# Optimization experiments

Hardware: AMD Instinct MI355X
Metric: run time of the kernel (lower is better)

Reference implementation:

```python
import jax, jax.numpy as jnp
import numpy as np

B, H, WD = 4, 1440, 1440      # batch, BEV grid (sparse_shape)
N, C, NB = 200000, 32, 3      # active voxels, channels, num basic blocks
EPS = 1e-3                    # BatchNorm1d eps in the module


def setup_inputs() -> dict:
    key = jax.random.key(0)
    ks = jax.random.split(key, 10)
    feats = jax.random.normal(ks[0], (N, C), jnp.float32)
    coords_b = jax.random.randint(ks[1], (N,), 0, B, dtype=jnp.int32)
    coords_y = jax.random.randint(ks[2], (N,), 0, H, dtype=jnp.int32)
    coords_x = jax.random.randint(ks[3], (N,), 0, WD, dtype=jnp.int32)
    # [block, conv(2), tap(3x3=9), Cin, Cout]; fan-in scaled init
    Wk = jax.random.normal(ks[4], (NB, 2, 9, C, C), jnp.float32) / np.sqrt(9 * C)
    bias = 0.01 * jax.random.normal(ks[5], (NB, 2, C), jnp.float32)
    gamma = 1.0 + 0.1 * jax.random.normal(ks[6], (NB, 2, C), jnp.float32)
    beta = 0.1 * jax.random.normal(ks[7], (NB, 2, C), jnp.float32)
    mean = 0.1 * jax.random.normal(ks[8], (NB, 2, C), jnp.float32)
    var = jax.random.uniform(ks[9], (NB, 2, C), jnp.float32, 0.5, 1.5)
    return dict(feats=feats, Wk=Wk, bias=bias, gamma=gamma, beta=beta,
                mean=mean, var=var, coords_b=coords_b, coords_y=coords_y,
                coords_x=coords_x)


def _build_rulebook(coords_b, coords_y, coords_x):
    # Dense hash: grid cell -> voxel row id (-1 if empty). Shared by all
    # submanifold convs in the stage (same indice_key in the original).
    idx_map = jnp.full((B, H, WD), -1, jnp.int32)
    idx_map = idx_map.at[coords_b, coords_y, coords_x].set(
        jnp.arange(N, dtype=jnp.int32))
    offs = jnp.array([(dy, dx) for dy in (-1, 0, 1) for dx in (-1, 0, 1)],
                     jnp.int32)                      # [9,2]
    ny = coords_y[None, :] + offs[:, 0:1]            # [9,N]
    nx = coords_x[None, :] + offs[:, 1:2]
    inb = (ny >= 0) & (ny < H) & (nx >= 0) & (nx < WD)
    nyc = jnp.clip(ny, 0, H - 1)
    nxc = jnp.clip(nx, 0, WD - 1)
    nidx = idx_map[jnp.broadcast_to(coords_b[None, :], (9, N)), nyc, nxc]
    mask = inb & (nidx >= 0)
    nidx = jnp.where(mask, nidx, 0)                  # safe gather index
    return nidx, mask[..., None].astype(jnp.float32)


def reference(feats, Wk, bias, gamma, beta, mean, var,
              coords_b, coords_y, coords_x):
    nidx, maskf = _build_rulebook(coords_b, coords_y, coords_x)

    def subm(x, w, b):
        # gather-GEMM-scatter submanifold 3x3 conv on active sites only
        g = x[nidx] * maskf                          # [9,N,Cin]
        return jnp.einsum('knc,kco->no', g, w) + b   # [N,Cout]

    def bn(x, g_, b_, m_, v_):
        return (x - m_) * jax.lax.rsqrt(v_ + EPS) * g_ + b_

    h = feats
    for i in range(NB):  # SparseBasicBlock stack (fixed small layer count)
        identity = h
        o = jax.nn.relu(bn(subm(h, Wk[i, 0], bias[i, 0]),
                           gamma[i, 0], beta[i, 0], mean[i, 0], var[i, 0]))
        o = bn(subm(o, Wk[i, 1], bias[i, 1]),
               gamma[i, 1], beta[i, 1], mean[i, 1], var[i, 1])
        h = jax.nn.relu(o + identity)
    return h
```

## Files before the change

kernel.cpp:

```cpp
#include <hip/hip_runtime.h>

#define NB_ 3
#define CB 4
#define CH 1440
#define CW 1440
#define NC 32
#define EPSV 1e-3f

typedef __attribute__((ext_vector_type(8))) short bf16x8;
typedef __attribute__((ext_vector_type(4))) float f32x4;

union U16 { uint4 u; bf16x8 v; };

__device__ __forceinline__ unsigned pk2(float a, float b) {
    unsigned ua = __float_as_uint(a), ub = __float_as_uint(b);
    ua += 0x7fffu + ((ua >> 16) & 1u);
    ub += 0x7fffu + ((ub >> 16) & 1u);
    return (ua >> 16) | (ub & 0xffff0000u);
}
__device__ __forceinline__ unsigned short f2b(float a) {
    unsigned u = __float_as_uint(a);
    u += 0x7fffu + ((u >> 16) & 1u);
    return (unsigned short)(u >> 16);
}
__device__ __forceinline__ float b2f(unsigned short s) {
    return __uint_as_float(((unsigned)s) << 16);
}

__global__ __launch_bounds__(256) void k_clear(
    const int* __restrict__ cb, const int* __restrict__ cy, const int* __restrict__ cx,
    int* __restrict__ idx_map, int n)
{
    int i = blockIdx.x * blockDim.x + threadIdx.x;
    if (i >= n) return;
    int b = cb[i], y = cy[i], x = cx[i];
    #pragma unroll
    for (int dy = -1; dy <= 1; ++dy) {
        int yy = y + dy;
        if (yy < 0 || yy >= CH) continue;
        #pragma unroll
        for (int dx = -1; dx <= 1; ++dx) {
            int xx = x + dx;
            if (xx < 0 || xx >= CW) continue;
            idx_map[((long)b * CH + yy) * CW + xx] = -1;
        }
    }
}

__global__ __launch_bounds__(256) void k_build_map(
    const int* __restrict__ cb, const int* __restrict__ cy, const int* __restrict__ cx,
    int* __restrict__ idx_map, int n)
{
    int i = blockIdx.x * blockDim.x + threadIdx.x;
    if (i < n) {
        long cell = ((long)cb[i] * CH + cy[i]) * CW + cx[i];
        atomicMax(&idx_map[cell], i);
    }
}

__global__ __launch_bounds__(256) void k_rulebook(
    const int* __restrict__ cb, const int* __restrict__ cy, const int* __restrict__ cx,
    const int* __restrict__ idx_map, int* __restrict__ nidx, int n)
{
    int i = blockIdx.x * blockDim.x + threadIdx.x;
    if (i >= n) return;
    int b = cb[i], y = cy[i], x = cx[i];
    nidx[4 * n + i] = idx_map[((long)b * CH + y) * CW + x];
    #pragma unroll
    for (int k = 0; k < 9; ++k) {
        if (k == 4) continue;
        int dy = k / 3 - 1, dx = k % 3 - 1;
        int ny = y + dy, nx = x + dx;
        int nb = -1;
        if (ny >= 0 && ny < CH && nx >= 0 && nx < CW)
            nb = idx_map[((long)b * CH + ny) * CW + nx];
        nidx[k * n + i] = nb;
    }
}

__global__ __launch_bounds__(256) void k_cvt(
    const float* __restrict__ f, unsigned short* __restrict__ b, int n32)
{
    int i = (blockIdx.x * 256 + threadIdx.x) * 8;
    if (i + 8 <= n32) {
        float4 a0 = *(const float4*)(f + i);
        float4 a1 = *(const float4*)(f + i + 4);
        uint4 r;
        r.x = pk2(a0.x, a0.y); r.y = pk2(a0.z, a0.w);
        r.z = pk2(a1.x, a1.y); r.w = pk2(a1.z, a1.w);
        *(uint4*)(b + i) = r;
    }
}

template<bool ADD_ID, bool F32OUT>
__global__ __launch_bounds__(256, 4) void k_conv(
    const unsigned short* __restrict__ in,
    const unsigned short* __restrict__ idn,
    void* __restrict__ outv,
    const float* __restrict__ W,
    const float* __restrict__ bias,
    const float* __restrict__ gamma, const float* __restrict__ beta,
    const float* __restrict__ mean, const float* __restrict__ var,
    const int* __restrict__ nidx, int n)
{
    __shared__ uint4 Bf[9 * 2 * 64];

    int tid = threadIdx.x;
    int l = tid & 63, wv = tid >> 6;

    for (int t = tid; t < 9 * 2 * 64; t += 256) {
        int lane = t & 63, nt = (t >> 6) & 1, k = t >> 7;
        int o = nt * 16 + (lane & 15);
        int c0 = (lane >> 4) * 8;
        const float* wp = W + k * 1024 + o;
        uint4 r;
        r.x = pk2(wp[(c0 + 0) * 32], wp[(c0 + 1) * 32]);
        r.y = pk2(wp[(c0 + 2) * 32], wp[(c0 + 3) * 32]);
        r.z = pk2(wp[(c0 + 4) * 32], wp[(c0 + 5) * 32]);
        r.w = pk2(wp[(c0 + 6) * 32], wp[(c0 + 7) * 32]);
        Bf[t] = r;
    }
    __syncthreads();

    int row = l & 15, grp = l >> 4;
    int o0 = row, o1 = row + 16;

    float sc0 = gamma[o0] * rsqrtf(var[o0] + EPSV);
    float sh0 = (bias[o0] - mean[o0]) * sc0 + beta[o0];
    float sc1 = gamma[o1] * rsqrtf(var[o1] + EPSV);
    float sh1 = (bias[o1] - mean[o1]) * sc1 + beta[o1];

    int ntile = (n + 15) >> 4;
    for (int tile = blockIdx.x * 4 + wv; tile < ntile; tile += gridDim.x * 4) {
        int p0 = tile << 4;
        int pr = p0 + row;
        bool rowok = pr < n;
        int prc = rowok ? pr : n - 1;

        int idxk[9];
        #pragma unroll
        for (int k = 0; k < 9; ++k) idxk[k] = nidx[(size_t)k * n + prc];

        bool act[9];
        U16 a[9];
        #pragma unroll
        for (int k = 0; k < 9; ++k) {
            act[k] = __any(idxk[k] >= 0);
            if (act[k]) {
                bool valid = rowok && (idxk[k] >= 0);
                int si = valid ? idxk[k] : 0;
                uint4 r = *(const uint4*)(in + (size_t)si * 32 + grp * 8);
                a[k].u.x = valid ? r.x : 0u;
                a[k].u.y = valid ? r.y : 0u;
                a[k].u.z = valid ? r.z : 0u;
                a[k].u.w = valid ? r.w : 0u;
            }
        }

        f32x4 acc0 = {0.f, 0.f, 0.f, 0.f};
        f32x4 acc1 = {0.f, 0.f, 0.f, 0.f};
        #pragma unroll
        for (int k = 0; k < 9; ++k) {
            if (act[k]) {
                U16 b0, b1;
                b0.u = Bf[(k * 2 + 0) * 64 + l];
                b1.u = Bf[(k * 2 + 1) * 64 + l];
                acc0 = __builtin_amdgcn_mfma_f32_16x16x32_bf16(a[k].v, b0.v, acc0, 0, 0, 0);
                acc1 = __builtin_amdgcn_mfma_f32_16x16x32_bf16(a[k].v, b1.v, acc1, 0, 0, 0);
            }
        }

        #pragma unroll
        for (int r = 0; r < 4; ++r) {
            int p = p0 + grp * 4 + r;
            if (p < n) {
                float y0 = acc0[r] * sc0 + sh0;
                float y1 = acc1[r] * sc1 + sh1;
                if (ADD_ID) {
                    y0 += b2f(idn[(size_t)p * 32 + o0]);
                    y1 += b2f(idn[(size_t)p * 32 + o1]);
                }
                y0 = fmaxf(y0, 0.f);
                y1 = fmaxf(y1, 0.f);
                if (F32OUT) {
                    ((float*)outv)[(size_t)p * 32 + o0] = y0;
                    ((float*)outv)[(size_t)p * 32 + o1] = y1;
                } else {
                    ((unsigned short*)outv)[(size_t)p * 32 + o0] = f2b(y0);
                    ((unsigned short*)outv)[(size_t)p * 32 + o1] = f2b(y1);
                }
            }
        }
    }
}

extern "C" void kernel_launch(void* const* d_in, const int* in_sizes, int n_in,
                              void* d_out, int out_size, void* d_ws, size_t ws_size,
                              hipStream_t stream)
{
    const float* feats = (const float*)d_in[0];
    const float* Wk    = (const float*)d_in[1];
    const float* bias  = (const float*)d_in[2];
    const float* gamma = (const float*)d_in[3];
    const float* beta  = (const float*)d_in[4];
    const float* mean  = (const float*)d_in[5];
    const float* var   = (const float*)d_in[6];
    const int* cb = (const int*)d_in[7];
    const int* cy = (const int*)d_in[8];
    const int* cx = (const int*)d_in[9];
    float* out = (float*)d_out;
    int n = in_sizes[0] / NC;

    char* ws = (char*)d_ws;
    int*            idx_map = (int*)(ws + 0);
    int*            nidx    = (int*)(ws + 33177600);
    unsigned short* xbf     = (unsigned short*)(ws + 40441600);
    unsigned short* tmpbf   = (unsigned short*)(ws + 53241600);
    unsigned short* hb      = (unsigned short*)(ws + 66041600);

    int blocks = (n + 255) / 256;
    k_clear<<<blocks, 256, 0, stream>>>(cb, cy, cx, idx_map, n);
    k_build_map<<<blocks, 256, 0, stream>>>(cb, cy, cx, idx_map, n);
    k_rulebook<<<blocks, 256, 0, stream>>>(cb, cy, cx, idx_map, nidx, n);
    k_cvt<<<(n * NC / 8 + 255) / 256, 256, 0, stream>>>(feats, xbf, n * NC);

    const int G = 1024;
    const int WSZ = 9 * 32 * 32;

    k_conv<false, false><<<G, 256, 0, stream>>>(xbf, nullptr, tmpbf,
        Wk + 0 * WSZ, bias + 0,  gamma + 0,  beta + 0,  mean + 0,  var + 0,  nidx, n);
    k_conv<true,  false><<<G, 256, 0, stream>>>(tmpbf, xbf, hb,
        Wk + 1 * WSZ, bias + 32, gamma + 32, beta + 32, mean + 32, var + 32, nidx, n);
    k_conv<false, false><<<G, 256, 0, stream>>>(hb, nullptr, tmpbf,
        Wk + 2 * WSZ, bias + 64, gamma + 64, beta + 64, mean + 64, var + 64, nidx, n);
    k_conv<true,  false><<<G, 256, 0, stream>>>(tmpbf, hb, xbf,
        Wk + 3 * WSZ, bias + 96, gamma + 96, beta + 96, mean + 96, var + 96, nidx, n);
    k_conv<false, false><<<G, 256, 0, stream>>>(xbf, nullptr, tmpbf,
        Wk + 4 * WSZ, bias + 128, gamma + 128, beta + 128, mean + 128, var + 128, nidx, n);
    k_conv<true,  true><<<G, 256, 0, stream>>>(tmpbf, xbf, out,
        Wk + 5 * WSZ, bias + 160, gamma + 160, beta + 160, mean + 160, var + 160, nidx, n);
}
```

Measured before the change: 149.5 us.

## Switch conv to 32x32x16 MFMA tiles with precomputed bf16 weights and byte offsets

Each conv kernel now works on 32-row tiles with the 32x32x16 bf16 MFMA instead of two 16x16x32 MFMAs on 16-row tiles. Weights for all six layers are converted to bf16 fragment layout once in a separate kernel and read from global memory, so each conv block no longer rebuilds them in shared memory. The rulebook now stores byte offsets, and a zero row appended to each feature buffer replaces the per-element select masking. The gathers are interleaved with the MFMAs. In exchange, the accumulator grows to 16 floats per lane, which raises register pressure, and the epilogue stores become more strided.

```diff
diff --git a/kernel.cpp b/kernel.cpp
--- a/kernel.cpp
+++ b/kernel.cpp
@@ -8,7 +8,7 @@
 #define EPSV 1e-3f
 
 typedef __attribute__((ext_vector_type(8))) short bf16x8;
-typedef __attribute__((ext_vector_type(4))) float f32x4;
+typedef __attribute__((ext_vector_type(16))) float f32x16;
 
 union U16 { uint4 u; bf16x8 v; };
 
@@ -60,12 +60,12 @@
 
 __global__ __launch_bounds__(256) void k_rulebook(
     const int* __restrict__ cb, const int* __restrict__ cy, const int* __restrict__ cx,
-    const int* __restrict__ idx_map, int* __restrict__ nidx, int n)
+    const int* __restrict__ idx_map, int* __restrict__ roff, int n)
 {
     int i = blockIdx.x * blockDim.x + threadIdx.x;
     if (i >= n) return;
     int b = cb[i], y = cy[i], x = cx[i];
-    nidx[4 * n + i] = idx_map[((long)b * CH + y) * CW + x];
+    roff[4 * n + i] = idx_map[((long)b * CH + y) * CW + x] * 64;
     #pragma unroll
     for (int k = 0; k < 9; ++k) {
         if (k == 4) continue;
@@ -74,7 +74,7 @@
         int nb = -1;
         if (ny >= 0 && ny < CH && nx >= 0 && nx < CW)
             nb = idx_map[((long)b * CH + ny) * CW + nx];
-        nidx[k * n + i] = nb;
+        roff[k * n + i] = (nb >= 0) ? nb * 64 : -1;
     }
 }
 
@@ -92,103 +92,90 @@
     }
 }
 
+__global__ __launch_bounds__(256) void k_wcvt(
+    const float* __restrict__ Wk, uint4* __restrict__ Bfg,
+    unsigned short* __restrict__ z0, unsigned short* __restrict__ z1,
+    unsigned short* __restrict__ z2)
+{
+    if (blockIdx.x == 0 && threadIdx.x < 12) {
+        uint4 z = make_uint4(0, 0, 0, 0);
+        int tt = threadIdx.x;
+        if (tt < 4)       ((uint4*)z0)[tt] = z;
+        else if (tt < 8)  ((uint4*)z1)[tt - 4] = z;
+        else              ((uint4*)z2)[tt - 8] = z;
+    }
+    int t = blockIdx.x * 256 + threadIdx.x;
+    if (t >= 6 * 9 * 2 * 64) return;
+    int l = t & 63, h = (t >> 6) & 1;
+    int rest = t >> 7;
+    int k = rest % 9, layer = rest / 9;
+    int o = l & 31;
+    int c0 = h * 16 + 8 * (l >> 5);
+    const float* wp = Wk + (size_t)layer * 9216 + k * 1024 + o;
+    uint4 r;
+    r.x = pk2(wp[(c0 + 0) * 32], wp[(c0 + 1) * 32]);
+    r.y = pk2(wp[(c0 + 2) * 32], wp[(c0 + 3) * 32]);
+    r.z = pk2(wp[(c0 + 4) * 32], wp[(c0 + 5) * 32]);
+    r.w = pk2(wp[(c0 + 6) * 32], wp[(c0 + 7) * 32]);
+    Bfg[t] = r;
+}
+
 template<bool ADD_ID, bool F32OUT>
 __global__ __launch_bounds__(256, 4) void k_conv(
     const unsigned short* __restrict__ in,
     const unsigned short* __restrict__ idn,
     void* __restrict__ outv,
-    const float* __restrict__ W,
+    const uint4* __restrict__ Bf,
     const float* __restrict__ bias,
     const float* __restrict__ gamma, const float* __restrict__ beta,
     const float* __restrict__ mean, const float* __restrict__ var,
-    const int* __restrict__ nidx, int n)
-{
-    __shared__ uint4 Bf[9 * 2 * 64];
-
-    int tid = threadIdx.x;
-    int l = tid & 63, wv = tid >> 6;
-
-    for (int t = tid; t < 9 * 2 * 64; t += 256) {
-        int lane = t & 63, nt = (t >> 6) & 1, k = t >> 7;
-        int o = nt * 16 + (lane & 15);
-        int c0 = (lane >> 4) * 8;
-        const float* wp = W + k * 1024 + o;
-        uint4 r;
-        r.x = pk2(wp[(c0 + 0) * 32], wp[(c0 + 1) * 32]);
-        r.y = pk2(wp[(c0 + 2) * 32], wp[(c0 + 3) * 32]);
-        r.z = pk2(wp[(c0 + 4) * 32], wp[(c0 + 5) * 32]);
-        r.w = pk2(wp[(c0 + 6) * 32], wp[(c0 + 7) * 32]);
-        Bf[t] = r;
-    }
-    __syncthreads();
-
-    int row = l & 15, grp = l >> 4;
-    int o0 = row, o1 = row + 16;
-
-    float sc0 = gamma[o0] * rsqrtf(var[o0] + EPSV);
-    float sh0 = (bias[o0] - mean[o0]) * sc0 + beta[o0];
-    float sc1 = gamma[o1] * rsqrtf(var[o1] + EPSV);
-    float sh1 = (bias[o1] - mean[o1]) * sc1 + beta[o1];
-
-    int ntile = (n + 15) >> 4;
+    const int* __restrict__ roff, int n)
+{
+    int l = threadIdx.x & 63, wv = threadIdx.x >> 6;
+    int q = l & 31, h5 = l >> 5;
+
+    float sc = gamma[q] * rsqrtf(var[q] + EPSV);
+    float sh = (bias[q] - mean[q]) * sc + beta[q];
+
+    const int zoff = n * 64;
+    const char* inB = (const char*)in;
+
+    int ntile = (n + 31) >> 5;
     for (int tile = blockIdx.x * 4 + wv; tile < ntile; tile += gridDim.x * 4) {
-        int p0 = tile << 4;
-        int pr = p0 + row;
+        int p0 = tile << 5;
+        int pr = p0 + q;
         bool rowok = pr < n;
         int prc = rowok ? pr : n - 1;
 
-        int idxk[9];
-        #pragma unroll
-        for (int k = 0; k < 9; ++k) idxk[k] = nidx[(size_t)k * n + prc];
-
-        bool act[9];
-        U16 a[9];
+        int rk[9];
+        #pragma unroll
+        for (int k = 0; k < 9; ++k) rk[k] = roff[(size_t)k * n + prc];
+
+        f32x16 acc = {0.f,0.f,0.f,0.f,0.f,0.f,0.f,0.f,0.f,0.f,0.f,0.f,0.f,0.f,0.f,0.f};
         #pragma unroll
         for (int k = 0; k < 9; ++k) {
-            act[k] = __any(idxk[k] >= 0);
-            if (act[k]) {
-                bool valid = rowok && (idxk[k] >= 0);
-                int si = valid ? idxk[k] : 0;
-                uint4 r = *(const uint4*)(in + (size_t)si * 32 + grp * 8);
-                a[k].u.x = valid ? r.x : 0u;
-                a[k].u.y = valid ? r.y : 0u;
-                a[k].u.z = valid ? r.z : 0u;
-                a[k].u.w = valid ? r.w : 0u;
+            if (__any(rk[k] >= 0)) {
+                int off = (rowok && rk[k] >= 0) ? rk[k] : zoff;
+                const char* ap = inB + off + h5 * 16;
+                U16 a0, a1, b0, b1;
+                a0.u = *(const uint4*)(ap);
+                a1.u = *(const uint4*)(ap + 32);
+                b0.u = Bf[(k * 2 + 0) * 64 + l];
+                b1.u = Bf[(k * 2 + 1) * 64 + l];
+                acc = __builtin_amdgcn_mfma_f32_32x32x16_bf16(a0.v, b0.v, acc, 0, 0, 0);
+                acc = __builtin_amdgcn_mfma_f32_32x32x16_bf16(a1.v, b1.v, acc, 0, 0, 0);
             }
         }
 
-        f32x4 acc0 = {0.f, 0.f, 0.f, 0.f};
-        f32x4 acc1 = {0.f, 0.f, 0.f, 0.f};
-        #pragma unroll
-        for (int k = 0; k < 9; ++k) {
-            if (act[k]) {
-                U16 b0, b1;
-                b0.u = Bf[(k * 2 + 0) * 64 + l];
-                b1.u = Bf[(k * 2 + 1) * 64 + l];
-                acc0 = __builtin_amdgcn_mfma_f32_16x16x32_bf16(a[k].v, b0.v, acc0, 0, 0, 0);
-                acc1 = __builtin_amdgcn_mfma_f32_16x16x32_bf16(a[k].v, b1.v, acc1, 0, 0, 0);
-            }
-        }
-
-        #pragma unroll
-        for (int r = 0; r < 4; ++r) {
-            int p = p0 + grp * 4 + r;
+        #pragma unroll
+        for (int r = 0; r < 16; ++r) {
+            int p = p0 + (r & 3) + 8 * (r >> 2) + 4 * h5;
             if (p < n) {
-                float y0 = acc0[r] * sc0 + sh0;
-                float y1 = acc1[r] * sc1 + sh1;
-                if (ADD_ID) {
-                    y0 += b2f(idn[(size_t)p * 32 + o0]);
-                    y1 += b2f(idn[(size_t)p * 32 + o1]);
-                }
-                y0 = fmaxf(y0, 0.f);
-                y1 = fmaxf(y1, 0.f);
-                if (F32OUT) {
-                    ((float*)outv)[(size_t)p * 32 + o0] = y0;
-                    ((float*)outv)[(size_t)p * 32 + o1] = y1;
-                } else {
-                    ((unsigned short*)outv)[(size_t)p * 32 + o0] = f2b(y0);
-                    ((unsigned short*)outv)[(size_t)p * 32 + o1] = f2b(y1);
-                }
+                float y = acc[r] * sc + sh;
+                if (ADD_ID) y += b2f(idn[(size_t)p * 32 + q]);
+                y = fmaxf(y, 0.f);
+                if (F32OUT) ((float*)outv)[(size_t)p * 32 + q] = y;
+                else ((unsigned short*)outv)[(size_t)p * 32 + q] = f2b(y);
             }
         }
     }
@@ -213,30 +200,33 @@
 
     char* ws = (char*)d_ws;
     int*            idx_map = (int*)(ws + 0);
-    int*            nidx    = (int*)(ws + 33177600);
-    unsigned short* xbf     = (unsigned short*)(ws + 40441600);
-    unsigned short* tmpbf   = (unsigned short*)(ws + 53241600);
-    unsigned short* hb      = (unsigned short*)(ws + 66041600);
+    int*            roff    = (int*)(ws + 33177600);
+    uint4*          Bfg     = (uint4*)(ws + 40377600);
+    unsigned short* xbf     = (unsigned short*)(ws + 40488192);
+    unsigned short* tmpbf   = (unsigned short*)(ws + 53288256);
+    unsigned short* hb      = (unsigned short*)(ws + 66088320);
 
     int blocks = (n + 255) / 256;
     k_clear<<<blocks, 256, 0, stream>>>(cb, cy, cx, idx_map, n);
     k_build_map<<<blocks, 256, 0, stream>>>(cb, cy, cx, idx_map, n);
-    k_rulebook<<<blocks, 256, 0, stream>>>(cb, cy, cx, idx_map, nidx, n);
+    k_rulebook<<<blocks, 256, 0, stream>>>(cb, cy, cx, idx_map, roff, n);
     k_cvt<<<(n * NC / 8 + 255) / 256, 256, 0, stream>>>(feats, xbf, n * NC);
+    k_wcvt<<<(6 * 9 * 2 * 64 + 255) / 256, 256, 0, stream>>>(
+        Wk, Bfg, xbf + (size_t)n * 32, tmpbf + (size_t)n * 32, hb + (size_t)n * 32);
 
     const int G = 1024;
-    const int WSZ = 9 * 32 * 32;
+    const int BSZ = 9 * 2 * 64;
 
     k_conv<false, false><<<G, 256, 0, stream>>>(xbf, nullptr, tmpbf,
-        Wk + 0 * WSZ, bias + 0,  gamma + 0,  beta + 0,  mean + 0,  var + 0,  nidx, n);
+        Bfg + 0 * BSZ, bias + 0,  gamma + 0,  beta + 0,  mean + 0,  var + 0,  roff, n);
     k_conv<true,  false><<<G, 256, 0, stream>>>(tmpbf, xbf, hb,
-        Wk + 1 * WSZ, bias + 32, gamma + 32, beta + 32, mean + 32, var + 32, nidx, n);
+        Bfg + 1 * BSZ, bias + 32, gamma + 32, beta + 32, mean + 32, var + 32, roff, n);
     k_conv<false, false><<<G, 256, 0, stream>>>(hb, nullptr, tmpbf,
-        Wk + 2 * WSZ, bias + 64, gamma + 64, beta + 64, mean + 64, var + 64, nidx, n);
+        Bfg + 2 * BSZ, bias + 64, gamma + 64, beta + 64, mean + 64, var + 64, roff, n);
     k_conv<true,  false><<<G, 256, 0, stream>>>(tmpbf, hb, xbf,
-        Wk + 3 * WSZ, bias + 96, gamma + 96, beta + 96, mean + 96, var + 96, nidx, n);
+        Bfg + 3 * BSZ, bias + 96, gamma + 96, beta + 96, mean + 96, var + 96, roff, n);
     k_conv<false, false><<<G, 256, 0, stream>>>(xbf, nullptr, tmpbf,
-        Wk + 4 * WSZ, bias + 128, gamma + 128, beta + 128, mean + 128, var + 128, nidx, n);
+        Bfg + 4 * BSZ, bias + 128, gamma + 128, beta + 128, mean + 128, var + 128, roff, n);
     k_conv<true,  true><<<G, 256, 0, stream>>>(tmpbf, xbf, out,
-        Wk + 5 * WSZ, bias + 160, gamma + 160, beta + 160, mean + 160, var + 160, nidx, n);
-}
+        Bfg + 5 * BSZ, bias + 160, gamma + 160, beta + 160, mean + 160, var + 160, roff, n);
+}
```

Result: no change. 148.6 us (-0.6%).
